# Optimization experiments

Measured on AMD Instinct MI355X. Metric: run time of the kernel, lower is better.

Reference implementation:

```python
import jax, jax.numpy as jnp
import numpy as np

B, S, D = 1, 1024, 2048          # batch, seq, hidden
H, KH, HD = 16, 16, 128          # heads, kv heads, head_dim
E, K, FI = 8, 4, 1408            # experts, top_k, moe_intermediate
FS = 5632                        # shared expert intermediate
WIN = 512                        # sliding window
THETA = 1.0e6                    # rope base
EPS = 1e-6                       # rmsnorm eps


def setup_inputs() -> dict:
    key = jax.random.key(0)
    ks = jax.random.split(key, 16)
    nrm = lambda k, shape: jax.random.normal(k, shape, jnp.float32) * 0.02
    return dict(
        hidden_states=jax.random.normal(ks[0], (B, S, D), jnp.float32),
        ln1_w=jnp.ones((D,), jnp.float32),
        ln2_w=jnp.ones((D,), jnp.float32),
        wq=nrm(ks[1], (D, H * HD)), bq=jnp.zeros((H * HD,), jnp.float32),
        wk=nrm(ks[2], (D, KH * HD)), bk=jnp.zeros((KH * HD,), jnp.float32),
        wv=nrm(ks[3], (D, KH * HD)), bv=jnp.zeros((KH * HD,), jnp.float32),
        wo=nrm(ks[4], (H * HD, D)),
        w_router=nrm(ks[5], (D, E)),
        w_gate_e=nrm(ks[6], (E, D, FI)),
        w_up_e=nrm(ks[7], (E, D, FI)),
        w_down_e=nrm(ks[8], (E, FI, D)),
        ws_gate=nrm(ks[9], (D, FS)),
        ws_up=nrm(ks[10], (D, FS)),
        ws_down=nrm(ks[11], (FS, D)),
        w_shared_gate=nrm(ks[12], (D, 1)),
    )


def _rms(h, w):
    v = jnp.mean(h * h, axis=-1, keepdims=True)
    return h * jax.lax.rsqrt(v + EPS) * w


def _rope(q, k):
    pos = jnp.arange(S, dtype=jnp.float32)
    inv = 1.0 / (THETA ** (jnp.arange(0, HD, 2, dtype=jnp.float32) / HD))
    ang = pos[:, None] * inv[None, :]                      # [S, HD/2]
    cos = jnp.concatenate([jnp.cos(ang)] * 2, -1)[None, :, None, :]
    sin = jnp.concatenate([jnp.sin(ang)] * 2, -1)[None, :, None, :]
    rot = lambda t: jnp.concatenate([-t[..., HD // 2:], t[..., :HD // 2]], -1)
    return q * cos + rot(q) * sin, k * cos + rot(k) * sin


def reference(hidden_states, ln1_w, ln2_w, wq, bq, wk, bk, wv, bv, wo,
              w_router, w_gate_e, w_up_e, w_down_e,
              ws_gate, ws_up, ws_down, w_shared_gate):
    x = hidden_states
    # --- sliding-window causal attention ---
    h = _rms(x, ln1_w)
    q = (h @ wq + bq).reshape(B, S, H, HD)
    k = (h @ wk + bk).reshape(B, S, KH, HD)
    v = (h @ wv + bv).reshape(B, S, KH, HD)
    q, k = _rope(q, k)
    scores = jnp.einsum('bqhd,bkhd->bhqk', q, k) * (HD ** -0.5)
    i = jnp.arange(S)[:, None]
    j = jnp.arange(S)[None, :]
    mask = (j <= i) & (i - j < WIN)                        # causal + window
    scores = jnp.where(mask[None, None], scores, jnp.finfo(scores.dtype).min)
    attn = jax.nn.softmax(scores, axis=-1)
    o = jnp.einsum('bhqk,bkhd->bqhd', attn, v).reshape(B, S, H * HD) @ wo
    x = x + o
    # --- sparse MoE block ---
    h = _rms(x, ln2_w)
    t = h.reshape(B * S, D)
    logits = (t @ w_router).astype(jnp.float32)
    probs = jax.nn.softmax(logits, axis=-1)                # [T, E]
    top_w, top_i = jax.lax.top_k(probs, K)                 # norm_topk_prob=False
    cw = jnp.zeros((B * S, E), probs.dtype).at[jnp.arange(B * S)[:, None], top_i].set(top_w)
    # routed experts (dense combine == gather/dispatch/grouped-GEMM/combine)
    g = jnp.einsum('td,edf->etf', t, w_gate_e)
    u = jnp.einsum('td,edf->etf', t, w_up_e)
    eo = jnp.einsum('etf,efd->etd', jax.nn.silu(g) * u, w_down_e)
    routed = jnp.einsum('te,etd->td', cw, eo)
    # shared expert with sigmoid gate
    shared = (jax.nn.silu(t @ ws_gate) * (t @ ws_up)) @ ws_down
    sgate = jax.nn.sigmoid(t @ w_shared_gate)              # [T, 1]
    moe = routed + sgate * shared
    return x + moe.reshape(B, S, D)
```

## Files before the change

kernel.cpp:

```cpp
#include <hip/hip_runtime.h>

#define S_ 1024
#define D_ 2048
#define H_ 16
#define HD_ 128
#define E_ 8
#define FI_ 1408
#define FS_ 5632
#define WIN_ 512
#define T_ 1024
#define QKVN 6144

typedef _Float16 f16;
typedef __attribute__((ext_vector_type(8))) _Float16 f16x8;
typedef __attribute__((ext_vector_type(4))) _Float16 f16x4;
typedef __attribute__((ext_vector_type(4))) float f32x4;

#define MFMA16(a, b, c) __builtin_amdgcn_mfma_f32_16x16x32_f16((a), (b), (c), 0, 0, 0)

__device__ __forceinline__ void gload16(const void* g, void* l) {
    __builtin_amdgcn_global_load_lds(
        (const __attribute__((address_space(1))) unsigned*)g,
        (__attribute__((address_space(3))) unsigned*)l, 16, 0, 0);
}

__global__ __launch_bounds__(256) void rmsnorm16_kernel(const float* __restrict__ x,
                                                        const float* __restrict__ w,
                                                        f16* __restrict__ out) {
    int t = blockIdx.x;
    const float* xr = x + (long)t * D_;
    int base = threadIdx.x * 8;
    float4 v0 = *(const float4*)(xr + base);
    float4 v1 = *(const float4*)(xr + base + 4);
    float ss = v0.x*v0.x + v0.y*v0.y + v0.z*v0.z + v0.w*v0.w
             + v1.x*v1.x + v1.y*v1.y + v1.z*v1.z + v1.w*v1.w;
    #pragma unroll
    for (int off = 1; off < 64; off <<= 1) ss += __shfl_xor(ss, off);
    __shared__ float red[4];
    if ((threadIdx.x & 63) == 0) red[threadIdx.x >> 6] = ss;
    __syncthreads();
    float tot = red[0] + red[1] + red[2] + red[3];
    float scale = rsqrtf(tot / (float)D_ + 1e-6f);
    float4 w0 = *(const float4*)(w + base);
    float4 w1 = *(const float4*)(w + base + 4);
    f16x8 o;
    o[0] = (f16)(v0.x*scale*w0.x); o[1] = (f16)(v0.y*scale*w0.y);
    o[2] = (f16)(v0.z*scale*w0.z); o[3] = (f16)(v0.w*scale*w0.w);
    o[4] = (f16)(v1.x*scale*w1.x); o[5] = (f16)(v1.y*scale*w1.y);
    o[6] = (f16)(v1.z*scale*w1.z); o[7] = (f16)(v1.w*scale*w1.w);
    *(f16x8*)(out + (long)t * D_ + base) = o;
}

__device__ __forceinline__ void tconv_body(const float* __restrict__ src,
                                           f16* __restrict__ dst,
                                           int K, int N, int mode) {
    int n0 = blockIdx.x * 64, k0 = blockIdx.y * 64;
    __shared__ f16 tile[64][72];
    int t = threadIdx.x, r = t >> 2, c4 = (t & 3) * 16;
    const float* sp = src + (long)(k0 + r) * N + n0 + c4;
    #pragma unroll
    for (int i = 0; i < 16; i += 4) {
        float4 v = *(const float4*)(sp + i);
        tile[c4 + i + 0][r] = (f16)v.x;
        tile[c4 + i + 1][r] = (f16)v.y;
        tile[c4 + i + 2][r] = (f16)v.z;
        tile[c4 + i + 3][r] = (f16)v.w;
    }
    __syncthreads();
    #pragma unroll
    for (int h = 0; h < 2; h++) {
        int v = t + h * 256;
        int nl = v >> 3, c8 = (v & 7) * 8;
        f16x8 vec = *(const f16x8*)&tile[nl][c8];
        int nr = n0 + nl;
        long orow = (mode == 0) ? nr
                  : ((long)(nr >> 4) * 32 + (nr & 15) + (mode == 2 ? 16 : 0));
        *(f16x8*)(dst + orow * K + k0 + c8) = vec;
    }
}

__global__ __launch_bounds__(256) void tconv_kernel(const float* __restrict__ src,
                                                    f16* __restrict__ dst,
                                                    int K, int N, long sSrc, long sDst) {
    tconv_body(src + (long)blockIdx.z * sSrc, dst + (long)blockIdx.z * sDst, K, N, 0);
}

__global__ __launch_bounds__(256) void tconv_qkvo_kernel(const float* __restrict__ wq,
                                                         const float* __restrict__ wk,
                                                         const float* __restrict__ wv,
                                                         const float* __restrict__ wo,
                                                         f16* __restrict__ dst) {
    int z = blockIdx.z;
    const float* src = (z == 0) ? wq : (z == 1) ? wk : (z == 2) ? wv : wo;
    tconv_body(src, dst + (long)z * 2048 * 2048, 2048, 2048, 0);
}

__global__ __launch_bounds__(256) void tconv_gu_kernel(const float* __restrict__ srcA,
                                                       const float* __restrict__ srcB,
                                                       f16* __restrict__ dst,
                                                       int K, int N, long sSrc, long sDst,
                                                       int zsplit) {
    int z = blockIdx.z;
    int e = (z < zsplit) ? z : z - zsplit;
    const float* src = ((z < zsplit) ? srcA : srcB) + (long)e * sSrc;
    tconv_body(src, dst + (long)e * sDst, K, N, (z < zsplit) ? 1 : 2);
}

template <int EPI, int MODE>
__global__ __launch_bounds__(256) void gemm16_kernel(
    const f16* __restrict__ Ag, const f16* __restrict__ BTg,
    void* Cg, const void* auxg,
    const int* __restrict__ tokidx, const int* __restrict__ cntv,
    const float* __restrict__ tw,
    int M, int N, int K, int lda, int ldb,
    long sA, long sB, long sC) {
    int z = blockIdx.z;
    const f16* A = Ag + (long)z * sA;
    const f16* BT = BTg + (long)z * sB;

    int nxy = gridDim.x * gridDim.y;
    int pid = blockIdx.y * gridDim.x + blockIdx.x;
    if ((nxy & 7) == 0) pid = (pid & 7) * (nxy >> 3) + (pid >> 3);
    int bx = pid / gridDim.y, by = pid % gridDim.y;
    int bm = by * 128, bn = bx * 128;

    int cnt = M;
    if (MODE >= 1) {
        cnt = cntv[z];
        if (bm >= cnt) return;
    }
    int tid = threadIdx.x, lane = tid & 63, wave = tid >> 6;
    int wm = (wave >> 1) * 64, wn = (wave & 1) * 64;

    __shared__ f16 As[128][64];
    __shared__ f16 Bs[128][64];

    f32x4 acc[4][4];
    #pragma unroll
    for (int i = 0; i < 4; i++)
        #pragma unroll
        for (int j = 0; j < 4; j++) acc[i][j] = (f32x4){0.f, 0.f, 0.f, 0.f};

    int srow8 = lane >> 3;
    int scol = ((lane & 7) ^ srow8) * 8;
    const f16* Abp[4];
    const f16* Bbp[4];
    #pragma unroll
    for (int i = 0; i < 4; i++) {
        int ra = bm + wave * 32 + i * 8 + srow8;
        long arow;
        if (MODE == 1) {
            int tok = (ra < cnt) ? tokidx[z * T_ + ra] : 0;
            arow = tok;
        } else {
            arow = ra;
        }
        Abp[i] = A + arow * (long)lda + scol;
        Bbp[i] = BT + (long)(bn + wave * 32 + i * 8 + srow8) * ldb + scol;
    }

    for (int k0 = 0; k0 < K; k0 += 64) {
        __syncthreads();
        #pragma unroll
        for (int i = 0; i < 4; i++) {
            gload16(Abp[i] + k0, &As[wave * 32 + i * 8][0]);
            gload16(Bbp[i] + k0, &Bs[wave * 32 + i * 8][0]);
        }
        __syncthreads();
        #pragma unroll
        for (int kk = 0; kk < 64; kk += 32) {
            f16x8 af[4], bf[4];
            #pragma unroll
            for (int mi = 0; mi < 4; mi++) {
                int r = wm + mi * 16 + (lane & 15);
                int c = ((kk >> 3) + (lane >> 4)) ^ (r & 7);
                af[mi] = *(const f16x8*)((const char*)&As[r][0] + (c << 4));
            }
            #pragma unroll
            for (int ni = 0; ni < 4; ni++) {
                int r = wn + ni * 16 + (lane & 15);
                int c = ((kk >> 3) + (lane >> 4)) ^ (r & 7);
                bf[ni] = *(const f16x8*)((const char*)&Bs[r][0] + (c << 4));
            }
            #pragma unroll
            for (int mi = 0; mi < 4; mi++)
                #pragma unroll
                for (int ni = 0; ni < 4; ni++)
                    acc[mi][ni] = MFMA16(af[mi], bf[ni], acc[mi][ni]);
        }
    }

    if (EPI == 5) {
        int half = N >> 1;
        #pragma unroll
        for (int mi = 0; mi < 4; mi++) {
            #pragma unroll
            for (int p = 0; p < 2; p++) {
                #pragma unroll
                for (int i = 0; i < 4; i++) {
                    int m = bm + wm + mi * 16 + (lane >> 4) * 4 + i;
                    int j = ((bn + wn) >> 1) + p * 16 + (lane & 15);
                    float g = acc[mi][2 * p][i];
                    float u = acc[mi][2 * p + 1][i];
                    ((f16*)Cg + (long)z * sC)[(long)m * half + j] =
                        (f16)(g / (1.f + __expf(-g)) * u);
                }
            }
        }
        return;
    }
    #pragma unroll
    for (int mi = 0; mi < 4; mi++) {
        #pragma unroll
        for (int ni = 0; ni < 4; ni++) {
            #pragma unroll
            for (int i = 0; i < 4; i++) {
                int m = bm + wm + mi * 16 + (lane >> 4) * 4 + i;
                int n = bn + wn + ni * 16 + (lane & 15);
                long idx = (long)m * N + n;
                float v = acc[mi][ni][i];
                if (EPI == 1) {
                    ((f16*)Cg)[idx] = (f16)(v + ((const float*)auxg)[n]);
                } else if (EPI == 4) {
                    ((float*)Cg + (long)z * sC)[idx] = v;
                } else if (EPI == 6) {
                    float wv = tw[z * T_ + m];
                    ((f16*)Cg + (long)z * sC)[idx] = (f16)(v * wv);
                }
            }
        }
    }
}

__global__ __launch_bounds__(256) void rope16_kernel(f16* __restrict__ qkv) {
    int s = blockIdx.x;
    float fs = (float)s;
    for (int p = threadIdx.x; p < H_ * 64; p += 256) {
        int h = p >> 6, j = p & 63;
        float inv = __expf(-(float)j * (13.815510557964274f / 64.f));
        float ang = fs * inv;
        float c = cosf(ang), sn = sinf(ang);
        long base = (long)s * QKVN + h * HD_ + j;
        float q1 = (float)qkv[base], q2 = (float)qkv[base + 64];
        qkv[base] = (f16)(q1 * c - q2 * sn);
        qkv[base + 64] = (f16)(q2 * c + q1 * sn);
        long kb = base + 2048;
        float k1 = (float)qkv[kb], k2 = (float)qkv[kb + 64];
        qkv[kb] = (f16)(k1 * c - k2 * sn);
        qkv[kb + 64] = (f16)(k2 * c + k1 * sn);
    }
}

__global__ __launch_bounds__(256) void attn16_kernel(const f16* __restrict__ qkv,
                                                     f16* __restrict__ Og) {
    int qt = blockIdx.x * 64;
    int head = blockIdx.y;
    int tid = threadIdx.x, lane = tid & 63, wave = tid >> 6;

    __shared__ f16 Ks[64][128];
    __shared__ f16 Vrow[64][128];
    __shared__ f16 VsT[128][64];
    __shared__ f16 Ps[4][16][64];

    int qr = qt + wave * 16 + (lane & 15);
    const f16* Qp = qkv + (long)qr * QKVN + head * HD_;
    f16x8 qf[4];
    #pragma unroll
    for (int kk = 0; kk < 4; kk++)
        qf[kk] = *(const f16x8*)(Qp + kk * 32 + (lane >> 4) * 8);

    f32x4 oacc[8];
    #pragma unroll
    for (int db = 0; db < 8; db++) oacc[db] = (f32x4){0.f, 0.f, 0.f, 0.f};
    float m_run[4] = {-1e30f, -1e30f, -1e30f, -1e30f};
    float l_run[4] = {0.f, 0.f, 0.f, 0.f};

    int k_lo = qt - (WIN_ - 1);
    if (k_lo < 0) k_lo = 0;
    k_lo &= ~63;

    for (int k0 = k_lo; k0 < qt + 64; k0 += 64) {
        __syncthreads();
        {
            int row = tid >> 2, cq = (tid & 3) * 32;
            const f16* Kp = qkv + (long)(k0 + row) * QKVN + 2048 + head * HD_ + cq;
            const f16* Vp = Kp + 2048;
            #pragma unroll
            for (int u = 0; u < 32; u += 8) {
                f16x8 tk = *(const f16x8*)(Kp + u);
                int co = ((cq + u) * 2) ^ ((row & 7) << 4);
                *(f16x8*)((char*)&Ks[row][0] + co) = tk;
                *(f16x8*)(&Vrow[row][cq + u]) = *(const f16x8*)(Vp + u);
            }
        }
        __syncthreads();
        {
            int d = tid >> 1, ks = (tid & 1) * 32;
            f16 tmp[32];
            #pragma unroll
            for (int j = 0; j < 32; j++) tmp[j] = Vrow[ks + j][d];
            #pragma unroll
            for (int u = 0; u < 32; u += 8) {
                int co = ((ks + u) * 2) ^ ((d & 7) << 4);
                f16x8 tv;
                #pragma unroll
                for (int j = 0; j < 8; j++) tv[j] = tmp[u + j];
                *(f16x8*)((char*)&VsT[d][0] + co) = tv;
            }
        }
        f32x4 sacc[4];
        #pragma unroll
        for (int cb = 0; cb < 4; cb++) sacc[cb] = (f32x4){0.f, 0.f, 0.f, 0.f};
        __builtin_amdgcn_s_setprio(1);
        #pragma unroll
        for (int kk = 0; kk < 4; kk++) {
            #pragma unroll
            for (int cb = 0; cb < 4; cb++) {
                int krow = cb * 16 + (lane & 15);
                int co = ((kk * 32 + (lane >> 4) * 8) * 2) ^ ((krow & 7) << 4);
                f16x8 kf = *(const f16x8*)((const char*)&Ks[krow][0] + co);
                sacc[cb] = MFMA16(qf[kk], kf, sacc[cb]);
            }
        }
        __builtin_amdgcn_s_setprio(0);
        float mtile[4] = {-1e30f, -1e30f, -1e30f, -1e30f};
        #pragma unroll
        for (int cb = 0; cb < 4; cb++) {
            #pragma unroll
            for (int i = 0; i < 4; i++) {
                int qi = qt + wave * 16 + (lane >> 4) * 4 + i;
                int kj = k0 + cb * 16 + (lane & 15);
                float s = sacc[cb][i] * 0.08838834764831845f;
                bool valid = (kj <= qi) && (qi - kj < WIN_);
                s = valid ? s : -1e30f;
                sacc[cb][i] = s;
                mtile[i] = fmaxf(mtile[i], s);
            }
        }
        #pragma unroll
        for (int i = 0; i < 4; i++) {
            float v = mtile[i];
            v = fmaxf(v, __shfl_xor(v, 1));
            v = fmaxf(v, __shfl_xor(v, 2));
            v = fmaxf(v, __shfl_xor(v, 4));
            v = fmaxf(v, __shfl_xor(v, 8));
            mtile[i] = v;
        }
        float pscale[4], lsum[4];
        #pragma unroll
        for (int i = 0; i < 4; i++) {
            float mnew = fmaxf(m_run[i], mtile[i]);
            pscale[i] = __expf(m_run[i] - mnew);
            m_run[i] = mnew;
            lsum[i] = 0.f;
        }
        #pragma unroll
        for (int cb = 0; cb < 4; cb++) {
            #pragma unroll
            for (int i = 0; i < 4; i++) {
                float mn = fmaxf(m_run[i], -1e20f);
                float p = __expf(sacc[cb][i] - mn);
                lsum[i] += p;
                int prow = (lane >> 4) * 4 + i;
                int pcol = cb * 16 + (lane & 15);
                int co = (pcol * 2) ^ ((prow & 7) << 4);
                *(f16*)((char*)&Ps[wave][prow][0] + co) = (f16)p;
            }
        }
        #pragma unroll
        for (int i = 0; i < 4; i++) {
            float v = lsum[i];
            v += __shfl_xor(v, 1);
            v += __shfl_xor(v, 2);
            v += __shfl_xor(v, 4);
            v += __shfl_xor(v, 8);
            l_run[i] = l_run[i] * pscale[i] + v;
        }
        #pragma unroll
        for (int db = 0; db < 8; db++)
            #pragma unroll
            for (int i = 0; i < 4; i++) oacc[db][i] *= pscale[i];
        __syncthreads();
        __builtin_amdgcn_s_setprio(1);
        #pragma unroll
        for (int ks = 0; ks < 2; ks++) {
            int prow = lane & 15;
            int co = ((ks * 32 + (lane >> 4) * 8) * 2) ^ ((prow & 7) << 4);
            f16x8 pf = *(const f16x8*)((const char*)&Ps[wave][prow][0] + co);
            #pragma unroll
            for (int db = 0; db < 8; db++) {
                int vrow2 = db * 16 + (lane & 15);
                int co2 = ((ks * 32 + (lane >> 4) * 8) * 2) ^ ((vrow2 & 7) << 4);
                f16x8 vf = *(const f16x8*)((const char*)&VsT[vrow2][0] + co2);
                oacc[db] = MFMA16(pf, vf, oacc[db]);
            }
        }
        __builtin_amdgcn_s_setprio(0);
    }
    #pragma unroll
    for (int db = 0; db < 8; db++) {
        #pragma unroll
        for (int i = 0; i < 4; i++) {
            int qi = qt + wave * 16 + (lane >> 4) * 4 + i;
            int d = db * 16 + (lane & 15);
            Og[(long)qi * D_ + head * HD_ + d] = (f16)(oacc[db][i] / l_run[i]);
        }
    }
}

__global__ __launch_bounds__(256) void postattn_kernel(
    const float* __restrict__ x, const float* __restrict__ p,
    const float* __restrict__ ln2, const float* __restrict__ wr,
    const float* __restrict__ wshg,
    float* __restrict__ x2, f16* __restrict__ h2,
    float* __restrict__ cw, float* __restrict__ sgate) {
    int t = blockIdx.x;
    int base = threadIdx.x * 8;
    long ro = (long)t * D_ + base;
    const long plane = (long)T_ * D_;
    float xv[8];
    #pragma unroll
    for (int j = 0; j < 8; j += 4) {
        float4 a = *(const float4*)(x + ro + j);
        float4 b = *(const float4*)(p + ro + j);
        float4 c = *(const float4*)(p + plane + ro + j);
        xv[j + 0] = a.x + b.x + c.x;
        xv[j + 1] = a.y + b.y + c.y;
        xv[j + 2] = a.z + b.z + c.z;
        xv[j + 3] = a.w + b.w + c.w;
    }
    *(float4*)(x2 + ro) = *(float4*)&xv[0];
    *(float4*)(x2 + ro + 4) = *(float4*)&xv[4];

    float ss = 0.f;
    #pragma unroll
    for (int j = 0; j < 8; j++) ss += xv[j] * xv[j];
    #pragma unroll
    for (int off = 1; off < 64; off <<= 1) ss += __shfl_xor(ss, off);
    __shared__ float red0[4];
    if ((threadIdx.x & 63) == 0) red0[threadIdx.x >> 6] = ss;
    __syncthreads();
    float scale = rsqrtf((red0[0] + red0[1] + red0[2] + red0[3]) / (float)D_ + 1e-6f);

    float part[9] = {0.f,0.f,0.f,0.f,0.f,0.f,0.f,0.f,0.f};
    f16x8 ho;
    #pragma unroll
    for (int j = 0; j < 8; j++) {
        int d = base + j;
        float hv = xv[j] * scale * ln2[d];
        ho[j] = (f16)hv;
        const float* wrow = wr + (long)d * E_;
        #pragma unroll
        for (int e = 0; e < 8; e++) part[e] += hv * wrow[e];
        part[8] += hv * wshg[d];
    }
    *(f16x8*)(h2 + ro) = ho;

    #pragma unroll
    for (int e = 0; e < 9; e++) {
        float v = part[e];
        #pragma unroll
        for (int off = 1; off < 64; off <<= 1) v += __shfl_xor(v, off);
        part[e] = v;
    }
    __shared__ float red[4][9];
    int lane = threadIdx.x & 63, wave = threadIdx.x >> 6;
    if (lane == 0)
        #pragma unroll
        for (int e = 0; e < 9; e++) red[wave][e] = part[e];
    __syncthreads();
    if (threadIdx.x == 0) {
        float logit[9];
        #pragma unroll
        for (int e = 0; e < 9; e++) logit[e] = red[0][e] + red[1][e] + red[2][e] + red[3][e];
        float mx = logit[0];
        #pragma unroll
        for (int e = 1; e < 8; e++) mx = fmaxf(mx, logit[e]);
        float pp[8], sum = 0.f;
        #pragma unroll
        for (int e = 0; e < 8; e++) { pp[e] = expf(logit[e] - mx); sum += pp[e]; }
        #pragma unroll
        for (int e = 0; e < 8; e++) pp[e] /= sum;
        float sel[8] = {0.f,0.f,0.f,0.f,0.f,0.f,0.f,0.f};
        float tmp[8];
        #pragma unroll
        for (int e = 0; e < 8; e++) tmp[e] = pp[e];
        for (int it = 0; it < 4; it++) {
            int best = 0;
            float bvv = tmp[0];
            #pragma unroll
            for (int e = 1; e < 8; e++)
                if (tmp[e] > bvv) { bvv = tmp[e]; best = e; }
            sel[best] = pp[best];
            tmp[best] = -1.f;
        }
        #pragma unroll
        for (int e = 0; e < 8; e++) cw[(long)e * T_ + t] = sel[e];
        sgate[t] = 1.f / (1.f + expf(-logit[8]));
    }
}

__global__ __launch_bounds__(512) void bucket_kernel(const float* __restrict__ cw,
                                                     int* __restrict__ cnt,
                                                     int* __restrict__ tokidx,
                                                     float* __restrict__ tw,
                                                     int* __restrict__ posmat) {
    int e = threadIdx.x >> 6, lane = threadIdx.x & 63;
    int count = 0;
    for (int base = 0; base < T_; base += 64) {
        int t = base + lane;
        float wv = cw[(long)e * T_ + t];
        unsigned long long m = __ballot(wv > 0.f);
        int pre = __popcll(m & ((1ull << lane) - 1ull));
        if (wv > 0.f) {
            int s = count + pre;
            tokidx[e * T_ + s] = t;
            tw[e * T_ + s] = wv;
            posmat[e * T_ + t] = s;
        }
        count += __popcll(m);
    }
    if (lane == 0) cnt[e] = count;
}

__global__ __launch_bounds__(256) void biascat_kernel(const float* bq, const float* bk,
                                                      const float* bv, float* bqkv) {
    int i = blockIdx.x * 256 + threadIdx.x;
    if (i < 2048) bqkv[i] = bq[i];
    else if (i < 4096) bqkv[i] = bk[i - 2048];
    else if (i < 6144) bqkv[i] = bv[i - 4096];
}

__global__ __launch_bounds__(256) void reduce4_kernel(const float* __restrict__ p,
                                                      float* __restrict__ out) {
    long total = (long)T_ * D_ / 4;
    for (long i = (long)blockIdx.x * 256 + threadIdx.x; i < total;
         i += (long)gridDim.x * 256) {
        float4 a = ((const float4*)p)[i];
        float4 b = ((const float4*)p)[i + total];
        float4 c = ((const float4*)p)[i + 2 * total];
        float4 d = ((const float4*)p)[i + 3 * total];
        float4 o;
        o.x = a.x + b.x + c.x + d.x; o.y = a.y + b.y + c.y + d.y;
        o.z = a.z + b.z + c.z + d.z; o.w = a.w + b.w + c.w + d.w;
        ((float4*)out)[i] = o;
    }
}

__global__ __launch_bounds__(256) void combine_kernel(
    const float* __restrict__ x2, const float* __restrict__ sho,
    const float* __restrict__ sg, const float* __restrict__ cw,
    const int* __restrict__ posmat, const f16* __restrict__ eo,
    float* __restrict__ out) {
    long total = (long)T_ * D_ / 4;
    for (long i = (long)blockIdx.x * 256 + threadIdx.x; i < total;
         i += (long)gridDim.x * 256) {
        int t = (int)(i >> 9);
        int c4 = (int)(i & 511) * 4;
        float4 a = ((const float4*)x2)[i];
        float4 s = ((const float4*)sho)[i];
        float g = sg[t];
        float r0 = a.x + g * s.x, r1 = a.y + g * s.y;
        float r2 = a.z + g * s.z, r3 = a.w + g * s.w;
        #pragma unroll
        for (int e = 0; e < 8; e++) {
            float w = cw[(long)e * T_ + t];
            if (w > 0.f) {
                int slot = posmat[(long)e * T_ + t];
                f16x4 v = *(const f16x4*)(eo + ((long)e * T_ + slot) * D_ + c4);
                r0 += (float)v[0]; r1 += (float)v[1];
                r2 += (float)v[2]; r3 += (float)v[3];
            }
        }
        float4 o; o.x = r0; o.y = r1; o.z = r2; o.w = r3;
        ((float4*)out)[i] = o;
    }
}

extern "C" void kernel_launch(void* const* d_in, const int* in_sizes, int n_in,
                              void* d_out, int out_size, void* d_ws, size_t ws_size,
                              hipStream_t stream) {
    const float* x    = (const float*)d_in[0];
    const float* ln1  = (const float*)d_in[1];
    const float* ln2  = (const float*)d_in[2];
    const float* wq   = (const float*)d_in[3];
    const float* bq   = (const float*)d_in[4];
    const float* wk   = (const float*)d_in[5];
    const float* bk   = (const float*)d_in[6];
    const float* wv   = (const float*)d_in[7];
    const float* bv   = (const float*)d_in[8];
    const float* wo   = (const float*)d_in[9];
    const float* wrt  = (const float*)d_in[10];
    const float* wge  = (const float*)d_in[11];
    const float* wue  = (const float*)d_in[12];
    const float* wde  = (const float*)d_in[13];
    const float* wsg  = (const float*)d_in[14];
    const float* wsu  = (const float*)d_in[15];
    const float* wsd  = (const float*)d_in[16];
    const float* wshg = (const float*)d_in[17];

    float* ws = (float*)d_ws;
    f16*   wT     = (f16*)ws;
    float* x2     = ws + 11534336;
    float* sho    = x2 + 2097152;
    float* bqkv   = sho + 2097152;
    float* cw     = bqkv + 6144;
    float* sg     = cw + 8192;
    int*   cnt    = (int*)(sg + 1024);
    int*   tokidx = cnt + 8;
    float* tw     = (float*)(tokidx + 8192);
    int*   posmat = (int*)(tw + 8192);
    f16*   h1     = (f16*)(posmat + 8192);
    f16*   h2     = (f16*)((float*)h1 + 1048576);
    float* pool   = (float*)h2 + 1048576;

    f16*   qkv     = (f16*)pool;
    float* woparts = pool + 3145728;
    f16*   sgb     = (f16*)pool;
    float* parts4  = pool + 2883584;
    f16*   Gg      = (f16*)pool;
    f16*   eo      = (f16*)(pool + 5767168);
    f16*   ao      = h1;

    dim3 blk(256);

    rmsnorm16_kernel<<<T_, blk, 0, stream>>>(x, ln1, h1);
    biascat_kernel<<<24, blk, 0, stream>>>(bq, bk, bv, bqkv);
    tconv_qkvo_kernel<<<dim3(32, 32, 4), blk, 0, stream>>>(wq, wk, wv, wo, wT);
    gemm16_kernel<1, 0><<<dim3(48, 8, 1), blk, 0, stream>>>(
        h1, wT, qkv, bqkv, nullptr, nullptr, nullptr,
        T_, QKVN, D_, 2048, 2048, 0, 0, 0);
    rope16_kernel<<<S_, blk, 0, stream>>>(qkv);
    attn16_kernel<<<dim3(16, 16), blk, 0, stream>>>(qkv, ao);
    gemm16_kernel<4, 0><<<dim3(16, 8, 2), blk, 0, stream>>>(
        ao, wT + 6144L * 2048, woparts, nullptr, nullptr, nullptr, nullptr,
        T_, D_, 1024, 2048, 2048, 1024, 1024, 2097152);
    postattn_kernel<<<T_, blk, 0, stream>>>(x, woparts, ln2, wrt, wshg, x2, h2, cw, sg);
    bucket_kernel<<<1, 512, 0, stream>>>(cw, cnt, tokidx, tw, posmat);

    tconv_gu_kernel<<<dim3(88, 32, 2), blk, 0, stream>>>(wsg, wsu, wT, 2048, 5632, 0, 0, 1);
    gemm16_kernel<5, 0><<<dim3(88, 8, 1), blk, 0, stream>>>(
        h2, wT, sgb, nullptr, nullptr, nullptr, nullptr,
        T_, 2 * FS_, D_, 2048, 2048, 0, 0, 0);
    tconv_kernel<<<dim3(32, 88, 1), blk, 0, stream>>>(wsd, wT, 5632, 2048, 0, 0);
    gemm16_kernel<4, 0><<<dim3(16, 8, 4), blk, 0, stream>>>(
        sgb, wT, parts4, nullptr, nullptr, nullptr, nullptr,
        T_, D_, 1408, 5632, 5632, 1408, 1408, 2097152);
    reduce4_kernel<<<512, blk, 0, stream>>>(parts4, sho);

    tconv_gu_kernel<<<dim3(22, 32, 8), blk, 0, stream>>>(
        wge, wue, wT, 2048, 1408, 2048L * 1408, 2816L * 2048, 4);
    gemm16_kernel<5, 1><<<dim3(22, 8, 4), blk, 0, stream>>>(
        h2, wT, Gg, nullptr, tokidx, cnt, nullptr,
        T_, 2 * FI_, D_, 2048, 2048, 0, 2816L * 2048, 1024L * 1408);
    tconv_gu_kernel<<<dim3(22, 32, 8), blk, 0, stream>>>(
        wge + 4L * 2048 * 1408, wue + 4L * 2048 * 1408, wT, 2048, 1408,
        2048L * 1408, 2816L * 2048, 4);
    gemm16_kernel<5, 1><<<dim3(22, 8, 4), blk, 0, stream>>>(
        h2, wT, Gg + 4L * 1024 * 1408, nullptr, tokidx + 4 * T_, cnt + 4, nullptr,
        T_, 2 * FI_, D_, 2048, 2048, 0, 2816L * 2048, 1024L * 1408);

    tconv_kernel<<<dim3(32, 22, 8), blk, 0, stream>>>(wde, wT, 1408, 2048,
                                                      1408L * 2048, 2048L * 1408);
    gemm16_kernel<6, 2><<<dim3(16, 8, 8), blk, 0, stream>>>(
        Gg, wT, eo, nullptr, nullptr, cnt, tw,
        T_, D_, 1408, 1408, 1408, 1024L * 1408, 2048L * 1408, 1024L * 2048);

    combine_kernel<<<1024, blk, 0, stream>>>(x2, sho, sg, cw, posmat, eo, (float*)d_out);
}
```

Measured before the change: 555.2 us.

## Use compacted expert block map for routed MoE GEMMs and merge expert halves

The bucket kernel now builds a compact list of (expert, M-block) pairs, and the routed gate/up and down GEMMs launch a 1-D grid over only the occupied blocks instead of a padded grid with early-exit blocks. The workspace is re-laid out with a larger weight buffer so all 8 experts' gate/up weights are converted in one launch, replacing the two half launches. This removes idle blocks and an extra launch pair, at the cost of a bigger workspace and a serial blkmap build on one thread.

```diff
diff --git a/kernel.cpp b/kernel.cpp
--- a/kernel.cpp
+++ b/kernel.cpp
@@ -111,24 +111,32 @@
     const f16* __restrict__ Ag, const f16* __restrict__ BTg,
     void* Cg, const void* auxg,
     const int* __restrict__ tokidx, const int* __restrict__ cntv,
-    const float* __restrict__ tw,
+    const float* __restrict__ tw, const int* __restrict__ blkmap,
     int M, int N, int K, int lda, int ldb,
     long sA, long sB, long sC) {
-    int z = blockIdx.z;
-    const f16* A = Ag + (long)z * sA;
-    const f16* BT = BTg + (long)z * sB;
-
     int nxy = gridDim.x * gridDim.y;
     int pid = blockIdx.y * gridDim.x + blockIdx.x;
     if ((nxy & 7) == 0) pid = (pid & 7) * (nxy >> 3) + (pid >> 3);
-    int bx = pid / gridDim.y, by = pid % gridDim.y;
-    int bm = by * 128, bn = bx * 128;
-
-    int cnt = M;
-    if (MODE >= 1) {
+    int bx, by;
+    if (MODE >= 3) { bx = pid % gridDim.x; by = pid / gridDim.x; }
+    else           { bx = pid / gridDim.y; by = pid % gridDim.y; }
+
+    int z, bm, cnt = M;
+    if (MODE >= 3) {
+        int nmb = blkmap[0];
+        if (by >= nmb) return;
+        z = blkmap[1 + by];
+        bm = blkmap[41 + by] * 128;
         cnt = cntv[z];
-        if (bm >= cnt) return;
-    }
+    } else {
+        z = blockIdx.z;
+        bm = by * 128;
+        if (MODE >= 1) { cnt = cntv[z]; if (bm >= cnt) return; }
+    }
+    int bn = bx * 128;
+    const f16* A = Ag + (long)z * sA;
+    const f16* BT = BTg + (long)z * sB;
+
     int tid = threadIdx.x, lane = tid & 63, wave = tid >> 6;
     int wm = (wave >> 1) * 64, wn = (wave & 1) * 64;
 
@@ -149,7 +157,7 @@
     for (int i = 0; i < 4; i++) {
         int ra = bm + wave * 32 + i * 8 + srow8;
         long arow;
-        if (MODE == 1) {
+        if (MODE == 1 || MODE == 3) {
             int tok = (ra < cnt) ? tokidx[z * T_ + ra] : 0;
             arow = tok;
         } else {
@@ -504,7 +512,9 @@
                                                      int* __restrict__ cnt,
                                                      int* __restrict__ tokidx,
                                                      float* __restrict__ tw,
-                                                     int* __restrict__ posmat) {
+                                                     int* __restrict__ posmat,
+                                                     int* __restrict__ blkmap) {
+    __shared__ int scnt[8];
     int e = threadIdx.x >> 6, lane = threadIdx.x & 63;
     int count = 0;
     for (int base = 0; base < T_; base += 64) {
@@ -520,7 +530,20 @@
         }
         count += __popcll(m);
     }
-    if (lane == 0) cnt[e] = count;
+    if (lane == 0) { cnt[e] = count; scnt[e] = count; }
+    __syncthreads();
+    if (threadIdx.x == 0) {
+        int nb = 0;
+        for (int ee = 0; ee < 8; ee++) {
+            int c = scnt[ee];
+            for (int mb = 0; mb * 128 < c; mb++) {
+                blkmap[1 + nb] = ee;
+                blkmap[41 + nb] = mb;
+                nb++;
+            }
+        }
+        blkmap[0] = nb;
+    }
 }
 
 __global__ __launch_bounds__(256) void biascat_kernel(const float* bq, const float* bk,
@@ -600,70 +623,64 @@
     const float* wshg = (const float*)d_in[17];
 
     float* ws = (float*)d_ws;
-    f16*   wT     = (f16*)ws;
-    float* x2     = ws + 11534336;
-    float* sho    = x2 + 2097152;
-    float* bqkv   = sho + 2097152;
-    float* cw     = bqkv + 6144;
-    float* sg     = cw + 8192;
-    int*   cnt    = (int*)(sg + 1024);
-    int*   tokidx = cnt + 8;
-    float* tw     = (float*)(tokidx + 8192);
-    int*   posmat = (int*)(tw + 8192);
-    f16*   h1     = (f16*)(posmat + 8192);
-    f16*   h2     = (f16*)((float*)h1 + 1048576);
-    float* pool   = (float*)h2 + 1048576;
-
-    f16*   qkv     = (f16*)pool;
-    float* woparts = pool + 3145728;
-    f16*   sgb     = (f16*)pool;
-    float* parts4  = pool + 2883584;
-    f16*   Gg      = (f16*)pool;
-    f16*   eo      = (f16*)(pool + 5767168);
+    float* x2     = ws;
+    float* sho    = ws + 2097152;
+    float* bqkv   = ws + 4194304;
+    float* cw     = ws + 4200448;
+    float* sg     = ws + 4208640;
+    int*   cnt    = (int*)(ws + 4209664);
+    int*   tokidx = (int*)(ws + 4209672);
+    float* tw     = ws + 4217864;
+    int*   posmat = (int*)(ws + 4226056);
+    int*   blkmap = (int*)(ws + 4234248);
+    f16*   h1     = (f16*)(ws + 4234376);
+    f16*   h2     = (f16*)(ws + 5282952);
+    float* big    = ws + 6331528;
+
+    f16*   wbig    = (f16*)big;
+    f16*   qkv     = (f16*)(big + 8388608);
+    float* woparts = big + 11534336;
+    f16*   sgb     = (f16*)(big + 11534336);
+    float* parts4  = big + 14417920;
+    f16*   Gg      = (f16*)(big + 23068672);
+    f16*   eo      = (f16*)(big + 11534336);
     f16*   ao      = h1;
 
     dim3 blk(256);
 
     rmsnorm16_kernel<<<T_, blk, 0, stream>>>(x, ln1, h1);
     biascat_kernel<<<24, blk, 0, stream>>>(bq, bk, bv, bqkv);
-    tconv_qkvo_kernel<<<dim3(32, 32, 4), blk, 0, stream>>>(wq, wk, wv, wo, wT);
+    tconv_qkvo_kernel<<<dim3(32, 32, 4), blk, 0, stream>>>(wq, wk, wv, wo, wbig);
     gemm16_kernel<1, 0><<<dim3(48, 8, 1), blk, 0, stream>>>(
-        h1, wT, qkv, bqkv, nullptr, nullptr, nullptr,
+        h1, wbig, qkv, bqkv, nullptr, nullptr, nullptr, nullptr,
         T_, QKVN, D_, 2048, 2048, 0, 0, 0);
     rope16_kernel<<<S_, blk, 0, stream>>>(qkv);
     attn16_kernel<<<dim3(16, 16), blk, 0, stream>>>(qkv, ao);
     gemm16_kernel<4, 0><<<dim3(16, 8, 2), blk, 0, stream>>>(
-        ao, wT + 6144L * 2048, woparts, nullptr, nullptr, nullptr, nullptr,
+        ao, wbig + 6144L * 2048, woparts, nullptr, nullptr, nullptr, nullptr, nullptr,
         T_, D_, 1024, 2048, 2048, 1024, 1024, 2097152);
     postattn_kernel<<<T_, blk, 0, stream>>>(x, woparts, ln2, wrt, wshg, x2, h2, cw, sg);
-    bucket_kernel<<<1, 512, 0, stream>>>(cw, cnt, tokidx, tw, posmat);
-
-    tconv_gu_kernel<<<dim3(88, 32, 2), blk, 0, stream>>>(wsg, wsu, wT, 2048, 5632, 0, 0, 1);
+    bucket_kernel<<<1, 512, 0, stream>>>(cw, cnt, tokidx, tw, posmat, blkmap);
+
+    tconv_gu_kernel<<<dim3(88, 32, 2), blk, 0, stream>>>(wsg, wsu, wbig, 2048, 5632, 0, 0, 1);
     gemm16_kernel<5, 0><<<dim3(88, 8, 1), blk, 0, stream>>>(
-        h2, wT, sgb, nullptr, nullptr, nullptr, nullptr,
+        h2, wbig, sgb, nullptr, nullptr, nullptr, nullptr, nullptr,
         T_, 2 * FS_, D_, 2048, 2048, 0, 0, 0);
-    tconv_kernel<<<dim3(32, 88, 1), blk, 0, stream>>>(wsd, wT, 5632, 2048, 0, 0);
+    tconv_kernel<<<dim3(32, 88, 1), blk, 0, stream>>>(wsd, wbig, 5632, 2048, 0, 0);
     gemm16_kernel<4, 0><<<dim3(16, 8, 4), blk, 0, stream>>>(
-        sgb, wT, parts4, nullptr, nullptr, nullptr, nullptr,
+        sgb, wbig, parts4, nullptr, nullptr, nullptr, nullptr, nullptr,
         T_, D_, 1408, 5632, 5632, 1408, 1408, 2097152);
     reduce4_kernel<<<512, blk, 0, stream>>>(parts4, sho);
 
-    tconv_gu_kernel<<<dim3(22, 32, 8), blk, 0, stream>>>(
-        wge, wue, wT, 2048, 1408, 2048L * 1408, 2816L * 2048, 4);
-    gemm16_kernel<5, 1><<<dim3(22, 8, 4), blk, 0, stream>>>(
-        h2, wT, Gg, nullptr, tokidx, cnt, nullptr,
+    tconv_gu_kernel<<<dim3(22, 32, 16), blk, 0, stream>>>(
+        wge, wue, wbig, 2048, 1408, 2048L * 1408, 2816L * 2048, 8);
+    gemm16_kernel<5, 3><<<dim3(22, 40, 1), blk, 0, stream>>>(
+        h2, wbig, Gg, nullptr, tokidx, cnt, nullptr, blkmap,
         T_, 2 * FI_, D_, 2048, 2048, 0, 2816L * 2048, 1024L * 1408);
-    tconv_gu_kernel<<<dim3(22, 32, 8), blk, 0, stream>>>(
-        wge + 4L * 2048 * 1408, wue + 4L * 2048 * 1408, wT, 2048, 1408,
-        2048L * 1408, 2816L * 2048, 4);
-    gemm16_kernel<5, 1><<<dim3(22, 8, 4), blk, 0, stream>>>(
-        h2, wT, Gg + 4L * 1024 * 1408, nullptr, tokidx + 4 * T_, cnt + 4, nullptr,
-        T_, 2 * FI_, D_, 2048, 2048, 0, 2816L * 2048, 1024L * 1408);
-
-    tconv_kernel<<<dim3(32, 22, 8), blk, 0, stream>>>(wde, wT, 1408, 2048,
+    tconv_kernel<<<dim3(32, 22, 8), blk, 0, stream>>>(wde, wbig, 1408, 2048,
                                                       1408L * 2048, 2048L * 1408);
-    gemm16_kernel<6, 2><<<dim3(16, 8, 8), blk, 0, stream>>>(
-        Gg, wT, eo, nullptr, nullptr, cnt, tw,
+    gemm16_kernel<6, 4><<<dim3(16, 40, 1), blk, 0, stream>>>(
+        Gg, wbig, eo, nullptr, nullptr, cnt, tw, blkmap,
         T_, D_, 1408, 1408, 1408, 1024L * 1408, 2048L * 1408, 1024L * 2048);
 
     combine_kernel<<<1024, blk, 0, stream>>>(x2, sho, sg, cw, posmat, eo, (float*)d_out);
```

Result: slower. 601.8 us (+8.4%).
